# Kernel tuning notes

Measured on AMD Instinct MI355X. Metric: run time of the kernel, lower is better.

The kernel has to match this reference:

```python
import jax, jax.numpy as jnp
import numpy as np

N, HR, HEADS = 1024, 2048, 4
C1 = HR // HEADS                      # 512 per-head dim, conv1
H2 = 2 * HEADS                        # 8 heads, conv2
C2 = (2 * HR) // (2 * HEADS)          # 512 per-head dim, conv2
EPS = 1e-5


def setup_inputs() -> dict:
    key = jax.random.key(0)
    ks = jax.random.split(key, 20)
    s1 = 1.0 / np.sqrt(N)
    s2 = 1.0 / np.sqrt(HR)
    f32 = jnp.float32
    d = {"x": jax.random.normal(ks[0], (N, N), f32)}
    # conv1 params (in=N, out=HR)
    d["q1_w"] = jax.random.normal(ks[1], (N, HR), f32) * s1
    d["q1_b"] = jnp.zeros((HR,), f32)
    d["k1_w"] = jax.random.normal(ks[2], (N, HR), f32) * s1
    d["k1_b"] = jnp.zeros((HR,), f32)
    d["v1_w"] = jax.random.normal(ks[3], (N, HR), f32) * s1
    d["v1_b"] = jnp.zeros((HR,), f32)
    d["e1_w"] = jax.random.normal(ks[4], (HR,), f32) * 0.1   # lin_edge (edge_dim=1, no bias)
    d["s1_w"] = jax.random.normal(ks[5], (N, HR), f32) * s1  # lin_skip
    d["s1_b"] = jnp.zeros((HR,), f32)
    d["gn1_gamma"] = jnp.ones((HR,), f32)
    d["gn1_beta"] = jnp.zeros((HR,), f32)
    d["gn1_ms"] = jnp.ones((HR,), f32)
    # conv2 params (in=HR, out=2*HR)
    d["q2_w"] = jax.random.normal(ks[6], (HR, 2 * HR), f32) * s2
    d["q2_b"] = jnp.zeros((2 * HR,), f32)
    d["k2_w"] = jax.random.normal(ks[7], (HR, 2 * HR), f32) * s2
    d["k2_b"] = jnp.zeros((2 * HR,), f32)
    d["v2_w"] = jax.random.normal(ks[8], (HR, 2 * HR), f32) * s2
    d["v2_b"] = jnp.zeros((2 * HR,), f32)
    d["e2_w"] = jax.random.normal(ks[9], (2 * HR,), f32) * 0.1
    d["s2_w"] = jax.random.normal(ks[10], (HR, 2 * HR), f32) * s2
    d["s2_b"] = jnp.zeros((2 * HR,), f32)
    d["gn2_gamma"] = jnp.ones((2 * HR,), f32)
    d["gn2_beta"] = jnp.zeros((2 * HR,), f32)
    d["gn2_ms"] = jnp.ones((2 * HR,), f32)
    return d


def _tconv(x, A, qw, qb, kw, kb, vw, vb, ew, sw, sb, H, Cd):
    # TransformerConv over fully-connected meshgrid graph; edge (r -> c) carries scalar A[r, c].
    # key_j/value_j get +A[r,c]*We; the edge term factors out so no [N,N,H,C] tensor is built.
    n = x.shape[0]
    q = (x @ qw + qb).reshape(n, H, Cd)   # targets c
    k = (x @ kw + kb).reshape(n, H, Cd)   # sources r
    v = (x @ vw + vb).reshape(n, H, Cd)
    We = ew.reshape(H, Cd)
    qk = jnp.einsum('chd,rhd->crh', q, k)                 # [N_tgt, N_src, H]
    qe = jnp.einsum('chd,hd->ch', q, We)                  # q_c . We per head
    logits = (qk + A.T[:, :, None] * qe[:, None, :]) / jnp.sqrt(jnp.float32(Cd))
    alpha = jax.nn.softmax(logits, axis=1)                # softmax over sources per target
    out = jnp.einsum('crh,rhd->chd', alpha, v)
    out = out + jnp.einsum('crh,rc->ch', alpha, A)[:, :, None] * We[None]
    return out.reshape(n, H * Cd) + x @ sw + sb           # root/skip connection


def _gnorm(x, gamma, beta, ms):
    # GraphNorm over a single graph: learnable mean-scale, per-feature stats across nodes.
    mu = x.mean(axis=0)
    out = x - ms * mu
    var = (out * out).mean(axis=0)
    return gamma * out * jax.lax.rsqrt(var + EPS) + beta


def reference(x, q1_w, q1_b, k1_w, k1_b, v1_w, v1_b, e1_w, s1_w, s1_b,
              gn1_gamma, gn1_beta, gn1_ms,
              q2_w, q2_b, k2_w, k2_b, v2_w, v2_b, e2_w, s2_w, s2_b,
              gn2_gamma, gn2_beta, gn2_ms):
    A = x  # edge attrs are x.view(-1, 1) over the meshgrid edge_index
    h1 = _tconv(x, A, q1_w, q1_b, k1_w, k1_b, v1_w, v1_b, e1_w, s1_w, s1_b, HEADS, C1)
    h1 = _gnorm(h1, gn1_gamma, gn1_beta, gn1_ms)
    h2 = _tconv(h1, A, q2_w, q2_b, k2_w, k2_b, v2_w, v2_b, e2_w, s2_w, s2_b, H2, C2)
    h2 = _gnorm(h2, gn2_gamma, gn2_beta, gn2_ms)
    return h2 / jnp.linalg.norm(h2, axis=1, keepdims=True)
```

## Files before the change

kernel.cpp:

```cpp
#include <hip/hip_runtime.h>
#include <math.h>

#define EPSV 1e-5f

typedef __attribute__((ext_vector_type(8))) short bf16x8;
typedef __attribute__((ext_vector_type(4))) float f32x4;

__device__ __forceinline__ unsigned short f2bf(float f) {
    unsigned int u = __float_as_uint(f);
    return (unsigned short)((u + 0x7fffu + ((u >> 16) & 1u)) >> 16);
}
__device__ __forceinline__ float b2f(unsigned short u) {
    return __uint_as_float(((unsigned int)u) << 16);
}

__device__ __forceinline__ void glds16(const unsigned short* g, unsigned short* l) {
    __builtin_amdgcn_global_load_lds(
        (const __attribute__((address_space(1))) void*)g,
        (__attribute__((address_space(3))) void*)l, 16, 0, 0);
}

template<int BIAS, int OUTBF>
__global__ __launch_bounds__(256) void gemm_bt(
    const unsigned short* __restrict__ A, const unsigned short* __restrict__ B,
    const float* __restrict__ bias, void* __restrict__ Cout,
    int K, int lda, int ldb, int ldc,
    long aH, long bH, long cH)
{
    __shared__ unsigned short As[4096];
    __shared__ unsigned short Bs[4096];
    const int tid = threadIdx.x;
    const int wid = tid >> 6, lane = tid & 63;
    const int bm = blockIdx.y * 128, bn = blockIdx.x * 128;
    A += (long)blockIdx.z * aH;
    B += (long)blockIdx.z * bH;

    const int wr = wid >> 1, wc = wid & 1;

    const int r0 = (wid << 4) + (lane >> 2);
    const int kq = (lane & 3) << 3;
    const unsigned short* gA0 = A + (long)(bm + r0) * lda + kq;
    const unsigned short* gA1 = gA0 + (long)64 * lda;
    const unsigned short* gB0 = B + (long)(bn + r0) * ldb + kq;
    const unsigned short* gB1 = gB0 + (long)64 * ldb;
    unsigned short* lA0 = &As[wid << 9];
    unsigned short* lA1 = &As[(wid << 9) + 2048];
    unsigned short* lB0 = &Bs[wid << 9];
    unsigned short* lB1 = &Bs[(wid << 9) + 2048];

    f32x4 acc[4][4];
    #pragma unroll
    for (int m = 0; m < 4; m++)
        #pragma unroll
        for (int n = 0; n < 4; n++) acc[m][n] = (f32x4){0.f, 0.f, 0.f, 0.f};

    const int fr = lane & 15;
    const int kb = (lane >> 4) << 3;
    const unsigned short* pA = &As[(wr * 64 + fr) * 32 + kb];
    const unsigned short* pB = &Bs[(wc * 64 + fr) * 32 + kb];

    for (int k0 = 0; k0 < K; k0 += 32) {
        glds16(gA0 + k0, lA0);
        glds16(gA1 + k0, lA1);
        glds16(gB0 + k0, lB0);
        glds16(gB1 + k0, lB1);
        __syncthreads();
        bf16x8 af[4], bfr[4];
        #pragma unroll
        for (int m = 0; m < 4; m++) af[m] = *(const bf16x8*)(pA + (m << 9));
        #pragma unroll
        for (int n = 0; n < 4; n++) bfr[n] = *(const bf16x8*)(pB + (n << 9));
        #pragma unroll
        for (int m = 0; m < 4; m++)
            #pragma unroll
            for (int n = 0; n < 4; n++)
                acc[m][n] = __builtin_amdgcn_mfma_f32_16x16x32_bf16(
                    af[m], bfr[n], acc[m][n], 0, 0, 0);
        __syncthreads();
    }

    const int er = (lane >> 4) << 2;
    const int ec = lane & 15;
    if (OUTBF) {
        unsigned short* C = (unsigned short*)Cout + (long)blockIdx.z * cH;
        #pragma unroll
        for (int m = 0; m < 4; m++)
            #pragma unroll
            for (int n = 0; n < 4; n++) {
                int col = bn + wc * 64 + n * 16 + ec;
                float bv = BIAS ? bias[col] : 0.f;
                #pragma unroll
                for (int j = 0; j < 4; j++) {
                    int row = bm + wr * 64 + m * 16 + er + j;
                    C[(long)row * ldc + col] = f2bf(acc[m][n][j] + bv);
                }
            }
    } else {
        float* C = (float*)Cout + (long)blockIdx.z * cH;
        #pragma unroll
        for (int m = 0; m < 4; m++)
            #pragma unroll
            for (int n = 0; n < 4; n++) {
                int col = bn + wc * 64 + n * 16 + ec;
                #pragma unroll
                for (int j = 0; j < 4; j++) {
                    int row = bm + wr * 64 + m * 16 + er + j;
                    C[(long)row * ldc + col] = acc[m][n][j];
                }
            }
    }
}

__global__ void f2b_kernel(const float* __restrict__ src, unsigned short* __restrict__ dst)
{
    long i = ((long)blockIdx.x * 256 + threadIdx.x) * 8;
    float4 a = *(const float4*)&src[i];
    float4 b = *(const float4*)&src[i + 4];
    unsigned short o[8] = { f2bf(a.x), f2bf(a.y), f2bf(a.z), f2bf(a.w),
                            f2bf(b.x), f2bf(b.y), f2bf(b.z), f2bf(b.w) };
    *(uint4*)&dst[i] = *(uint4*)o;
}

__global__ void transpose_f2b(const float* __restrict__ src, unsigned short* __restrict__ dst,
                              int ldsrc, int Kdim)
{
    __shared__ float t[32][33];
    int f0 = blockIdx.x * 32, k0 = blockIdx.y * 32;
    int tx = threadIdx.x, ty = threadIdx.y;
    #pragma unroll
    for (int i = 0; i < 4; i++)
        t[ty + i * 8][tx] = src[(long)(k0 + ty + i * 8) * ldsrc + f0 + tx];
    __syncthreads();
    #pragma unroll
    for (int i = 0; i < 4; i++)
        dst[(long)(f0 + ty + i * 8) * Kdim + k0 + tx] = f2bf(t[tx][ty + i * 8]);
}

__global__ void transpose_b2b(const unsigned short* __restrict__ src,
                              unsigned short* __restrict__ dst, int ldsrc, int Cd)
{
    __shared__ unsigned short t[32][33];
    int h = blockIdx.z;
    int d0 = blockIdx.x * 32, r0 = blockIdx.y * 32;
    int tx = threadIdx.x, ty = threadIdx.y;
    #pragma unroll
    for (int i = 0; i < 4; i++)
        t[ty + i * 8][tx] = src[(long)(r0 + ty + i * 8) * ldsrc + h * Cd + d0 + tx];
    __syncthreads();
    #pragma unroll
    for (int i = 0; i < 4; i++)
        dst[(long)h * Cd * 1024 + (long)(d0 + ty + i * 8) * 1024 + r0 + tx] = t[tx][ty + i * 8];
}

__global__ void concat4(const float* __restrict__ a, const float* __restrict__ b,
                        const float* __restrict__ c, const float* __restrict__ d,
                        float* __restrict__ o, int F)
{
    int i = blockIdx.x * 256 + threadIdx.x;
    const float* s = (i < F) ? a : (i < 2 * F) ? b : (i < 3 * F) ? c : d;
    o[i] = s[i & (F - 1)];
}

__global__ void transpose1024(const float* __restrict__ in, float* __restrict__ out)
{
    __shared__ float t[32][33];
    int bx = blockIdx.x * 32, by = blockIdx.y * 32;
    #pragma unroll
    for (int i = 0; i < 32; i += 8)
        t[threadIdx.y + i][threadIdx.x] = in[(long)(by + threadIdx.y + i) * 1024 + bx + threadIdx.x];
    __syncthreads();
    #pragma unroll
    for (int i = 0; i < 32; i += 8)
        out[(long)(bx + threadIdx.y + i) * 1024 + by + threadIdx.x] = t[threadIdx.x][threadIdx.y + i];
}

__global__ __launch_bounds__(256) void compute_qe_b(
    const unsigned short* __restrict__ q, const float* __restrict__ ew,
    float* __restrict__ qe, int H, int Cd, int ldq)
{
    int gw = (blockIdx.x * 256 + threadIdx.x) >> 6;
    int lane = threadIdx.x & 63;
    int c = gw / H, h = gw - c * H;
    const unsigned short* qr = q + (long)c * ldq + h * Cd;
    const float* w = ew + h * Cd;
    int d = lane * 8;
    ushort4 u0 = *(const ushort4*)&qr[d];
    ushort4 u1 = *(const ushort4*)&qr[d + 4];
    float4 w0 = *(const float4*)&w[d];
    float4 w1 = *(const float4*)&w[d + 4];
    float s = b2f(u0.x) * w0.x + b2f(u0.y) * w0.y + b2f(u0.z) * w0.z + b2f(u0.w) * w0.w
            + b2f(u1.x) * w1.x + b2f(u1.y) * w1.y + b2f(u1.z) * w1.z + b2f(u1.w) * w1.w;
    #pragma unroll
    for (int o = 32; o; o >>= 1) s += __shfl_xor(s, o);
    if (lane == 0) qe[c * H + h] = s;
}

__global__ __launch_bounds__(256) void softmax_edge(
    const float* __restrict__ S, const float* __restrict__ xT,
    const float* __restrict__ qe, float* __restrict__ aw,
    unsigned short* __restrict__ ab, int H, float inv_sqrt_d)
{
    const int c = blockIdx.x, h = blockIdx.y, tid = threadIdx.x;
    const float* row = S + ((long)h * 1024 + c) * 1024;
    unsigned short* arow = ab + ((long)h * 1024 + c) * 1024;
    const float* xc = xT + (long)c * 1024;
    const float qeh = qe[c * H + h] * inv_sqrt_d;
    float l[4], xv[4];
    float mx = -1e30f;
    #pragma unroll
    for (int i = 0; i < 4; i++) {
        int r = tid + i * 256;
        xv[i] = xc[r];
        l[i] = row[r] * inv_sqrt_d + xv[i] * qeh;
        mx = fmaxf(mx, l[i]);
    }
    __shared__ float red[8];
    #pragma unroll
    for (int o = 32; o; o >>= 1) mx = fmaxf(mx, __shfl_xor(mx, o));
    if ((tid & 63) == 0) red[tid >> 6] = mx;
    __syncthreads();
    mx = fmaxf(fmaxf(red[0], red[1]), fmaxf(red[2], red[3]));
    __syncthreads();
    float e[4], se = 0.f, sa = 0.f;
    #pragma unroll
    for (int i = 0; i < 4; i++) {
        e[i] = __expf(l[i] - mx);
        se += e[i];
        sa += e[i] * xv[i];
    }
    #pragma unroll
    for (int o = 32; o; o >>= 1) { se += __shfl_xor(se, o); sa += __shfl_xor(sa, o); }
    if ((tid & 63) == 0) { red[tid >> 6] = se; red[4 + (tid >> 6)] = sa; }
    __syncthreads();
    se = red[0] + red[1] + red[2] + red[3];
    sa = red[4] + red[5] + red[6] + red[7];
    float inv = 1.f / se;
    #pragma unroll
    for (int i = 0; i < 4; i++) arow[tid + i * 256] = f2bf(e[i] * inv);
    if (tid == 0) aw[c * H + h] = sa * inv;
}

__global__ void combine2(float* __restrict__ out, const unsigned short* __restrict__ skipb,
                         int ldskip, const float* __restrict__ aw, const float* __restrict__ ew,
                         int F, int H)
{
    long idx = ((long)blockIdx.x * 256 + threadIdx.x) * 4;
    int c = (int)(idx / F), f = (int)(idx % F);
    int h = f >> 9;
    float a = aw[c * H + h];
    ushort4 sk = *(const ushort4*)&skipb[(long)c * ldskip + f];
    float4 o = *(float4*)&out[idx];
    float4 w = *(const float4*)&ew[f];
    o.x += b2f(sk.x) + a * w.x; o.y += b2f(sk.y) + a * w.y;
    o.z += b2f(sk.z) + a * w.z; o.w += b2f(sk.w) + a * w.w;
    *(float4*)&out[idx] = o;
}

__global__ void col_stats1(const float* __restrict__ X, float* __restrict__ ps,
                           float* __restrict__ ps2, int F)
{
    int f = blockIdx.x * 256 + threadIdx.x;
    int r0 = blockIdx.y * 32;
    float s = 0.f, s2 = 0.f;
    for (int r = r0; r < r0 + 32; r++) {
        float v = X[(long)r * F + f];
        s += v; s2 += v * v;
    }
    ps [(long)blockIdx.y * F + f] = s;
    ps2[(long)blockIdx.y * F + f] = s2;
}

__global__ void col_stats2(const float* __restrict__ ps, const float* __restrict__ ps2,
    const float* __restrict__ ms, float* __restrict__ msmu, float* __restrict__ rs, int F)
{
    int f = blockIdx.x * 256 + threadIdx.x;
    float s = 0.f, s2 = 0.f;
    for (int ch = 0; ch < 32; ch++) { s += ps[(long)ch * F + f]; s2 += ps2[(long)ch * F + f]; }
    float m  = s  * (1.f / 1024.f);
    float m2 = s2 * (1.f / 1024.f);
    float a = ms[f] * m;
    msmu[f] = a;
    float var = m2 - 2.f * a * m + a * a;
    rs[f] = rsqrtf(var + EPSV);
}

__global__ void gnorm_apply(float* __restrict__ X, const float* __restrict__ msmu,
    const float* __restrict__ rs, const float* __restrict__ g, const float* __restrict__ b, int F)
{
    long idx = ((long)blockIdx.x * 256 + threadIdx.x) * 4;
    int f = (int)(idx % F);
    float4 v = *(float4*)&X[idx];
    v.x = g[f+0] * (v.x - msmu[f+0]) * rs[f+0] + b[f+0];
    v.y = g[f+1] * (v.y - msmu[f+1]) * rs[f+1] + b[f+1];
    v.z = g[f+2] * (v.z - msmu[f+2]) * rs[f+2] + b[f+2];
    v.w = g[f+3] * (v.w - msmu[f+3]) * rs[f+3] + b[f+3];
    *(float4*)&X[idx] = v;
}

__global__ __launch_bounds__(256) void l2norm_rows(float* __restrict__ X, int F)
{
    const int r = blockIdx.x, tid = threadIdx.x;
    float* row = X + (long)r * F;
    float s = 0.f;
    for (int f = tid * 4; f < F; f += 1024) {
        float4 v = *(const float4*)&row[f];
        s += v.x*v.x + v.y*v.y + v.z*v.z + v.w*v.w;
    }
    __shared__ float red[4];
    #pragma unroll
    for (int o = 32; o; o >>= 1) s += __shfl_xor(s, o);
    if ((tid & 63) == 0) red[tid >> 6] = s;
    __syncthreads();
    s = red[0] + red[1] + red[2] + red[3];
    float inv = rsqrtf(s);
    for (int f = tid * 4; f < F; f += 1024) {
        float4 v = *(const float4*)&row[f];
        v.x *= inv; v.y *= inv; v.z *= inv; v.w *= inv;
        *(float4*)&row[f] = v;
    }
}

typedef unsigned short u16;

static inline void launch_gemm(hipStream_t st, const u16* A, const u16* B, const float* bias,
                               void* C, int M, int N, int K, int lda, int ldb, int ldc,
                               int nz, long aH, long bH, long cH, bool outbf)
{
    dim3 g(N / 128, M / 128, nz), b(256);
    if (outbf) {
        if (bias) gemm_bt<1,1><<<g, b, 0, st>>>(A, B, bias, C, K, lda, ldb, ldc, aH, bH, cH);
        else      gemm_bt<0,1><<<g, b, 0, st>>>(A, B, bias, C, K, lda, ldb, ldc, aH, bH, cH);
    } else {
        gemm_bt<0,0><<<g, b, 0, st>>>(A, B, bias, C, K, lda, ldb, ldc, aH, bH, cH);
    }
}

extern "C" void kernel_launch(void* const* d_in, const int* in_sizes, int n_in,
                              void* d_out, int out_size, void* d_ws, size_t ws_size,
                              hipStream_t stream)
{
    const float* x    = (const float*)d_in[0];
    const float* q1w  = (const float*)d_in[1];  const float* q1b = (const float*)d_in[2];
    const float* k1w  = (const float*)d_in[3];  const float* k1b = (const float*)d_in[4];
    const float* v1w  = (const float*)d_in[5];  const float* v1b = (const float*)d_in[6];
    const float* e1w  = (const float*)d_in[7];
    const float* s1w  = (const float*)d_in[8];  const float* s1b = (const float*)d_in[9];
    const float* gn1g = (const float*)d_in[10]; const float* gn1b = (const float*)d_in[11];
    const float* gn1ms= (const float*)d_in[12];
    const float* q2w  = (const float*)d_in[13]; const float* q2b = (const float*)d_in[14];
    const float* k2w  = (const float*)d_in[15]; const float* k2b = (const float*)d_in[16];
    const float* v2w  = (const float*)d_in[17]; const float* v2b = (const float*)d_in[18];
    const float* e2w  = (const float*)d_in[19];
    const float* s2w  = (const float*)d_in[20]; const float* s2b = (const float*)d_in[21];
    const float* gn2g = (const float*)d_in[22]; const float* gn2b = (const float*)d_in[23];
    const float* gn2ms= (const float*)d_in[24];
    float* out = (float*)d_out;

    char* W = (char*)d_ws;
    float* xT    = (float*)W;               W += (long)1024 * 1024 * 4;
    u16*   xb    = (u16*)W;                 W += (long)1024 * 1024 * 2;
    float* h1    = (float*)W;               W += (long)1024 * 2048 * 4;
    u16*   h1b   = (u16*)W;                 W += (long)1024 * 2048 * 2;
    u16*   projC = (u16*)W;                 W += (long)1024 * 16384 * 2;
    char*  R     = W;                       W += (long)8192 * 2048 * 2;
    u16*   WT    = (u16*)R;
    float* S     = (float*)R;
    u16*   ab    = (u16*)W;                 W += (long)8 * 1024 * 1024 * 2;
    u16*   VT    = (u16*)W;                 W += (long)8 * 512 * 1024 * 2;
    float* bc    = (float*)W;               W += 16384 * 4;
    float* qe    = (float*)W;               W += 8192 * 4;
    float* aw    = (float*)W;               W += 8192 * 4;
    float* ps    = (float*)W;               W += (long)32 * 4096 * 4;
    float* ps2   = (float*)W;               W += (long)32 * 4096 * 4;
    float* msmu  = (float*)W;               W += 4096 * 4;
    float* rs    = (float*)W;               W += 4096 * 4;

    const float isd = 1.0f / sqrtf(512.0f);

    transpose1024<<<dim3(32, 32), dim3(32, 8), 0, stream>>>(x, xT);
    f2b_kernel<<<512, 256, 0, stream>>>(x, xb);

    {
        const int F = 2048, K = 1024, H = 4;
        transpose_f2b<<<dim3(64, 32), dim3(32, 8), 0, stream>>>(q1w, WT + (long)0 * F * K, F, K);
        transpose_f2b<<<dim3(64, 32), dim3(32, 8), 0, stream>>>(k1w, WT + (long)1 * F * K, F, K);
        transpose_f2b<<<dim3(64, 32), dim3(32, 8), 0, stream>>>(v1w, WT + (long)2 * F * K, F, K);
        transpose_f2b<<<dim3(64, 32), dim3(32, 8), 0, stream>>>(s1w, WT + (long)3 * F * K, F, K);
        concat4<<<32, 256, 0, stream>>>(q1b, k1b, v1b, s1b, bc, F);
        launch_gemm(stream, xb, WT, bc, projC, 1024, 4 * F, K, K, K, 4 * F, 1, 0, 0, 0, true);

        compute_qe_b<<<1024, 256, 0, stream>>>(projC, e1w, qe, H, 512, 4 * F);
        launch_gemm(stream, projC, projC + F, nullptr, S, 1024, 1024, 512,
                    4 * F, 4 * F, 1024, H, 512, 512, (long)1024 * 1024, false);
        softmax_edge<<<dim3(1024, H), 256, 0, stream>>>(S, xT, qe, aw, ab, H, isd);
        transpose_b2b<<<dim3(16, 32, H), dim3(32, 8), 0, stream>>>(projC + 2 * F, VT, 4 * F, 512);
        launch_gemm(stream, ab, VT, nullptr, h1, 1024, 512, 1024,
                    1024, 1024, F, H, (long)1024 * 1024, (long)512 * 1024, 512, false);
        combine2<<<2048, 256, 0, stream>>>(h1, projC + 3 * F, 4 * F, aw, e1w, F, H);

        col_stats1<<<dim3(F / 256, 32), 256, 0, stream>>>(h1, ps, ps2, F);
        col_stats2<<<F / 256, 256, 0, stream>>>(ps, ps2, gn1ms, msmu, rs, F);
        gnorm_apply<<<(int)((long)1024 * F / 4 / 256), 256, 0, stream>>>(h1, msmu, rs, gn1g, gn1b, F);
    }
    f2b_kernel<<<1024, 256, 0, stream>>>(h1, h1b);

    {
        const int F = 4096, K = 2048, H = 8;
        concat4<<<64, 256, 0, stream>>>(q2b, k2b, v2b, s2b, bc, F);
        transpose_f2b<<<dim3(128, 64), dim3(32, 8), 0, stream>>>(q2w, WT + (long)0 * F * K, F, K);
        transpose_f2b<<<dim3(128, 64), dim3(32, 8), 0, stream>>>(k2w, WT + (long)1 * F * K, F, K);
        launch_gemm(stream, h1b, WT, bc, projC, 1024, 2 * F, K, K, K, 4 * F, 1, 0, 0, 0, true);
        transpose_f2b<<<dim3(128, 64), dim3(32, 8), 0, stream>>>(v2w, WT + (long)0 * F * K, F, K);
        transpose_f2b<<<dim3(128, 64), dim3(32, 8), 0, stream>>>(s2w, WT + (long)1 * F * K, F, K);
        launch_gemm(stream, h1b, WT, bc + 2 * F, projC + 2 * F, 1024, 2 * F, K, K, K, 4 * F, 1, 0, 0, 0, true);

        compute_qe_b<<<2048, 256, 0, stream>>>(projC, e2w, qe, H, 512, 4 * F);
        launch_gemm(stream, projC, projC + F, nullptr, S, 1024, 1024, 512,
                    4 * F, 4 * F, 1024, H, 512, 512, (long)1024 * 1024, false);
        softmax_edge<<<dim3(1024, H), 256, 0, stream>>>(S, xT, qe, aw, ab, H, isd);
        transpose_b2b<<<dim3(16, 32, H), dim3(32, 8), 0, stream>>>(projC + 2 * F, VT, 4 * F, 512);
        launch_gemm(stream, ab, VT, nullptr, out, 1024, 512, 1024,
                    1024, 1024, F, H, (long)1024 * 1024, (long)512 * 1024, 512, false);
        combine2<<<4096, 256, 0, stream>>>(out, projC + 3 * F, 4 * F, aw, e2w, F, H);

        col_stats1<<<dim3(F / 256, 32), 256, 0, stream>>>(out, ps, ps2, F);
        col_stats2<<<F / 256, 256, 0, stream>>>(ps, ps2, gn2ms, msmu, rs, F);
        gnorm_apply<<<(int)((long)1024 * F / 4 / 256), 256, 0, stream>>>(out, msmu, rs, gn2g, gn2b, F);
    }
    l2norm_rows<<<1024, 256, 0, stream>>>(out, 4096);
}
```

Measured before the change: 585.7 us.

## Replace GEMM with 256x128 triple-buffered swizzled kernel and fuse elementwise passes

Replaces the 128x128 single-buffered bf16 GEMM with a 512-thread 128x256 tile kernel. It uses BK=64, three LDS buffers with global_load_lds prefetch, XOR swizzling and raw barriers and waitcnts. Several small kernels are fused: the combine step goes into the PV GEMM epilogue, qe into the softmax, gnorm into the bf16 cast and into the L2 norm, the x transpose into the cast, and the four weight transposes into one launch. The goal is higher MFMA utilisation and fewer launches and memory passes, at the cost of large LDS use and hand-tuned synchronisation that could be fragile.

Result: faster. 472.4 us (-19.3%).

```diff
diff --git a/kernel.cpp b/kernel.cpp
--- a/kernel.cpp
+++ b/kernel.cpp
@@ -5,95 +5,147 @@
 
 typedef __attribute__((ext_vector_type(8))) short bf16x8;
 typedef __attribute__((ext_vector_type(4))) float f32x4;
-
-__device__ __forceinline__ unsigned short f2bf(float f) {
+typedef unsigned short u16;
+
+__device__ __forceinline__ u16 f2bf(float f) {
     unsigned int u = __float_as_uint(f);
-    return (unsigned short)((u + 0x7fffu + ((u >> 16) & 1u)) >> 16);
-}
-__device__ __forceinline__ float b2f(unsigned short u) {
+    return (u16)((u + 0x7fffu + ((u >> 16) & 1u)) >> 16);
+}
+__device__ __forceinline__ float b2f(u16 u) {
     return __uint_as_float(((unsigned int)u) << 16);
 }
 
-__device__ __forceinline__ void glds16(const unsigned short* g, unsigned short* l) {
+__device__ __forceinline__ void glds16(const u16* g, u16* l) {
     __builtin_amdgcn_global_load_lds(
         (const __attribute__((address_space(1))) void*)g,
         (__attribute__((address_space(3))) void*)l, 16, 0, 0);
 }
 
-template<int BIAS, int OUTBF>
-__global__ __launch_bounds__(256) void gemm_bt(
-    const unsigned short* __restrict__ A, const unsigned short* __restrict__ B,
+#define BARRIER() asm volatile("s_barrier" ::: "memory")
+#define VMCNT(n)  asm volatile("s_waitcnt vmcnt(" #n ")" ::: "memory")
+
+template<int BIAS, int OUTBF, int PVEPI>
+__global__ __launch_bounds__(512, 2) void gemm256(
+    const u16* __restrict__ A, const u16* __restrict__ B,
     const float* __restrict__ bias, void* __restrict__ Cout,
-    int K, int lda, int ldb, int ldc,
-    long aH, long bH, long cH)
-{
-    __shared__ unsigned short As[4096];
-    __shared__ unsigned short Bs[4096];
+    int K, int lda, int ldb, int ldc, long aH, long bH, long cH,
+    const u16* __restrict__ skipb, int ldsk,
+    const float* __restrict__ aw, const float* __restrict__ ew, int H)
+{
+    __shared__ __align__(16) u16 LB[3 * 24576];
     const int tid = threadIdx.x;
     const int wid = tid >> 6, lane = tid & 63;
-    const int bm = blockIdx.y * 128, bn = blockIdx.x * 128;
-    A += (long)blockIdx.z * aH;
-    B += (long)blockIdx.z * bH;
-
-    const int wr = wid >> 1, wc = wid & 1;
-
-    const int r0 = (wid << 4) + (lane >> 2);
-    const int kq = (lane & 3) << 3;
-    const unsigned short* gA0 = A + (long)(bm + r0) * lda + kq;
-    const unsigned short* gA1 = gA0 + (long)64 * lda;
-    const unsigned short* gB0 = B + (long)(bn + r0) * ldb + kq;
-    const unsigned short* gB1 = gB0 + (long)64 * ldb;
-    unsigned short* lA0 = &As[wid << 9];
-    unsigned short* lA1 = &As[(wid << 9) + 2048];
-    unsigned short* lB0 = &Bs[wid << 9];
-    unsigned short* lB1 = &Bs[(wid << 9) + 2048];
-
+    const int wm = wid >> 2, wn = wid & 3;
+    const int fr = lane & 15, g = lane >> 4;
+    const int bm = blockIdx.y * 128, bn = blockIdx.x * 256;
+    if (PVEPI) { A += (long)(bn >> 9) * aH; }
+    else       { A += (long)blockIdx.z * aH; B += (long)blockIdx.z * bH; }
+
+    const int srow = tid >> 3;
+    const int kx = ((tid & 7) ^ (srow & 7)) << 3;
+    const u16* gA = A + (long)(bm + srow) * lda + kx;
+    const u16* gB = B + (long)(bn + srow) * ldb + kx;
+
+#define STAGEA(dst, tt) do { const u16* s_ = gA + ((long)(tt) << 6); \
+    u16* d_ = (dst) + (wid << 9); \
+    glds16(s_, d_); glds16(s_ + (long)64 * lda, d_ + 4096); } while (0)
+#define STAGEB(dst, tt) do { const u16* s_ = gB + ((long)(tt) << 6); \
+    u16* d_ = (dst) + 8192 + (wid << 9); \
+    glds16(s_, d_); \
+    glds16(s_ + (long)64 * ldb, d_ + 4096); \
+    glds16(s_ + (long)128 * ldb, d_ + 8192); \
+    glds16(s_ + (long)192 * ldb, d_ + 12288); } while (0)
+
+    const int q0 = ((0 + g) ^ (fr & 7)) << 3;
+    const int q1 = ((4 + g) ^ (fr & 7)) << 3;
+    bf16x8 am[4], bq[4];
     f32x4 acc[4][4];
     #pragma unroll
     for (int m = 0; m < 4; m++)
         #pragma unroll
         for (int n = 0; n < 4; n++) acc[m][n] = (f32x4){0.f, 0.f, 0.f, 0.f};
 
-    const int fr = lane & 15;
-    const int kb = (lane >> 4) << 3;
-    const unsigned short* pA = &As[(wr * 64 + fr) * 32 + kb];
-    const unsigned short* pB = &Bs[(wc * 64 + fr) * 32 + kb];
-
-    for (int k0 = 0; k0 < K; k0 += 32) {
-        glds16(gA0 + k0, lA0);
-        glds16(gA1 + k0, lA1);
-        glds16(gB0 + k0, lB0);
-        glds16(gB1 + k0, lB1);
-        __syncthreads();
-        bf16x8 af[4], bfr[4];
-        #pragma unroll
-        for (int m = 0; m < 4; m++) af[m] = *(const bf16x8*)(pA + (m << 9));
-        #pragma unroll
-        for (int n = 0; n < 4; n++) bfr[n] = *(const bf16x8*)(pB + (n << 9));
-        #pragma unroll
-        for (int m = 0; m < 4; m++)
-            #pragma unroll
-            for (int n = 0; n < 4; n++)
-                acc[m][n] = __builtin_amdgcn_mfma_f32_16x16x32_bf16(
-                    af[m], bfr[n], acc[m][n], 0, 0, 0);
-        __syncthreads();
-    }
-
-    const int er = (lane >> 4) << 2;
-    const int ec = lane & 15;
-    if (OUTBF) {
-        unsigned short* C = (unsigned short*)Cout + (long)blockIdx.z * cH;
+#define RD8(bp, qq) do { \
+    const u16* pa_ = (bp) + ((wm << 6) + fr) * 64; \
+    const u16* pb_ = (bp) + 8192 + ((wn << 6) + fr) * 64; \
+    am[0] = *(const bf16x8*)(pa_ + (qq)); \
+    am[1] = *(const bf16x8*)(pa_ + 1024 + (qq)); \
+    am[2] = *(const bf16x8*)(pa_ + 2048 + (qq)); \
+    am[3] = *(const bf16x8*)(pa_ + 3072 + (qq)); \
+    bq[0] = *(const bf16x8*)(pb_ + (qq)); \
+    bq[1] = *(const bf16x8*)(pb_ + 1024 + (qq)); \
+    bq[2] = *(const bf16x8*)(pb_ + 2048 + (qq)); \
+    bq[3] = *(const bf16x8*)(pb_ + 3072 + (qq)); } while (0)
+
+#define MFMA16() do { __builtin_amdgcn_s_setprio(1); \
+    _Pragma("unroll") for (int m_ = 0; m_ < 4; m_++) \
+    _Pragma("unroll") for (int n_ = 0; n_ < 4; n_++) \
+        acc[m_][n_] = __builtin_amdgcn_mfma_f32_16x16x32_bf16(am[m_], bq[n_], acc[m_][n_], 0, 0, 0); \
+    __builtin_amdgcn_s_setprio(0); } while (0)
+
+    u16* pr = LB;
+    u16* pn = LB + 24576;
+    u16* ps = LB + 49152;
+
+    STAGEA(pr, 0); STAGEB(pr, 0);
+    STAGEA(pn, 1); STAGEB(pn, 1);
+    VMCNT(6);
+    BARRIER();
+
+    const int NT = K >> 6;
+    for (int t = 0; t < NT - 2; ++t) {
+        RD8(pr, q0);
+        STAGEA(ps, t + 2);
+        BARRIER();
+        MFMA16();
+        BARRIER();
+        RD8(pr, q1);
+        STAGEB(ps, t + 2);
+        VMCNT(6);
+        BARRIER();
+        MFMA16();
+        BARRIER();
+        u16* tmp = pr; pr = pn; pn = ps; ps = tmp;
+    }
+    RD8(pr, q0); BARRIER(); MFMA16(); BARRIER();
+    RD8(pr, q1);
+    VMCNT(0);
+    BARRIER();
+    MFMA16();
+    RD8(pn, q0); MFMA16();
+    RD8(pn, q1); MFMA16();
+
+    const int er = g << 2;
+    const int crow0 = bm + (wm << 6);
+    const int ccol0 = bn + (wn << 6);
+    if (PVEPI) {
+        float* C = (float*)Cout;
         #pragma unroll
         for (int m = 0; m < 4; m++)
             #pragma unroll
             for (int n = 0; n < 4; n++) {
-                int col = bn + wc * 64 + n * 16 + ec;
+                int f = ccol0 + (n << 4) + fr;
+                int h = f >> 9;
+                float ewf = ew[f];
+                #pragma unroll
+                for (int j = 0; j < 4; j++) {
+                    int row = crow0 + (m << 4) + er + j;
+                    C[(long)row * ldc + f] = acc[m][n][j]
+                        + b2f(skipb[(long)row * ldsk + f])
+                        + aw[row * H + h] * ewf;
+                }
+            }
+    } else if (OUTBF) {
+        u16* C = (u16*)Cout + (long)blockIdx.z * cH;
+        #pragma unroll
+        for (int m = 0; m < 4; m++)
+            #pragma unroll
+            for (int n = 0; n < 4; n++) {
+                int col = ccol0 + (n << 4) + fr;
                 float bv = BIAS ? bias[col] : 0.f;
                 #pragma unroll
-                for (int j = 0; j < 4; j++) {
-                    int row = bm + wr * 64 + m * 16 + er + j;
-                    C[(long)row * ldc + col] = f2bf(acc[m][n][j] + bv);
-                }
+                for (int j = 0; j < 4; j++)
+                    C[(long)(crow0 + (m << 4) + er + j) * ldc + col] = f2bf(acc[m][n][j] + bv);
             }
     } else {
         float* C = (float*)Cout + (long)blockIdx.z * cH;
@@ -101,29 +153,41 @@
         for (int m = 0; m < 4; m++)
             #pragma unroll
             for (int n = 0; n < 4; n++) {
-                int col = bn + wc * 64 + n * 16 + ec;
+                int col = ccol0 + (n << 4) + fr;
                 #pragma unroll
-                for (int j = 0; j < 4; j++) {
-                    int row = bm + wr * 64 + m * 16 + er + j;
-                    C[(long)row * ldc + col] = acc[m][n][j];
-                }
+                for (int j = 0; j < 4; j++)
+                    C[(long)(crow0 + (m << 4) + er + j) * ldc + col] = acc[m][n][j];
             }
     }
-}
-
-__global__ void f2b_kernel(const float* __restrict__ src, unsigned short* __restrict__ dst)
-{
-    long i = ((long)blockIdx.x * 256 + threadIdx.x) * 8;
-    float4 a = *(const float4*)&src[i];
-    float4 b = *(const float4*)&src[i + 4];
-    unsigned short o[8] = { f2bf(a.x), f2bf(a.y), f2bf(a.z), f2bf(a.w),
-                            f2bf(b.x), f2bf(b.y), f2bf(b.z), f2bf(b.w) };
-    *(uint4*)&dst[i] = *(uint4*)o;
-}
-
-__global__ void transpose_f2b(const float* __restrict__ src, unsigned short* __restrict__ dst,
-                              int ldsrc, int Kdim)
-{
+#undef STAGEA
+#undef STAGEB
+#undef RD8
+#undef MFMA16
+}
+
+__global__ void xprep(const float* __restrict__ in, float* __restrict__ outT,
+                      u16* __restrict__ outB)
+{
+    __shared__ float t[32][33];
+    int bx = blockIdx.x * 32, by = blockIdx.y * 32;
+    #pragma unroll
+    for (int i = 0; i < 32; i += 8) {
+        float v = in[(long)(by + threadIdx.y + i) * 1024 + bx + threadIdx.x];
+        t[threadIdx.y + i][threadIdx.x] = v;
+        outB[(long)(by + threadIdx.y + i) * 1024 + bx + threadIdx.x] = f2bf(v);
+    }
+    __syncthreads();
+    #pragma unroll
+    for (int i = 0; i < 32; i += 8)
+        outT[(long)(bx + threadIdx.y + i) * 1024 + by + threadIdx.x] = t[threadIdx.x][threadIdx.y + i];
+}
+
+__global__ void wtrans4(const float* s0, const float* s1, const float* s2, const float* s3,
+                        u16* __restrict__ dst, int ldsrc, int Kdim, long dstride)
+{
+    int which = blockIdx.z;
+    const float* src = which == 0 ? s0 : which == 1 ? s1 : which == 2 ? s2 : s3;
+    dst += (long)which * dstride;
     __shared__ float t[32][33];
     int f0 = blockIdx.x * 32, k0 = blockIdx.y * 32;
     int tx = threadIdx.x, ty = threadIdx.y;
@@ -136,10 +200,10 @@
         dst[(long)(f0 + ty + i * 8) * Kdim + k0 + tx] = f2bf(t[tx][ty + i * 8]);
 }
 
-__global__ void transpose_b2b(const unsigned short* __restrict__ src,
-                              unsigned short* __restrict__ dst, int ldsrc, int Cd)
-{
-    __shared__ unsigned short t[32][33];
+__global__ void transpose_b2b(const u16* __restrict__ src,
+                              u16* __restrict__ dst, int ldsrc, int Cd)
+{
+    __shared__ u16 t[32][33];
     int h = blockIdx.z;
     int d0 = blockIdx.x * 32, r0 = blockIdx.y * 32;
     int tx = threadIdx.x, ty = threadIdx.y;
@@ -161,60 +225,36 @@
     o[i] = s[i & (F - 1)];
 }
 
-__global__ void transpose1024(const float* __restrict__ in, float* __restrict__ out)
-{
-    __shared__ float t[32][33];
-    int bx = blockIdx.x * 32, by = blockIdx.y * 32;
-    #pragma unroll
-    for (int i = 0; i < 32; i += 8)
-        t[threadIdx.y + i][threadIdx.x] = in[(long)(by + threadIdx.y + i) * 1024 + bx + threadIdx.x];
-    __syncthreads();
-    #pragma unroll
-    for (int i = 0; i < 32; i += 8)
-        out[(long)(bx + threadIdx.y + i) * 1024 + by + threadIdx.x] = t[threadIdx.x][threadIdx.y + i];
-}
-
-__global__ __launch_bounds__(256) void compute_qe_b(
-    const unsigned short* __restrict__ q, const float* __restrict__ ew,
-    float* __restrict__ qe, int H, int Cd, int ldq)
-{
-    int gw = (blockIdx.x * 256 + threadIdx.x) >> 6;
-    int lane = threadIdx.x & 63;
-    int c = gw / H, h = gw - c * H;
-    const unsigned short* qr = q + (long)c * ldq + h * Cd;
-    const float* w = ew + h * Cd;
-    int d = lane * 8;
-    ushort4 u0 = *(const ushort4*)&qr[d];
-    ushort4 u1 = *(const ushort4*)&qr[d + 4];
-    float4 w0 = *(const float4*)&w[d];
-    float4 w1 = *(const float4*)&w[d + 4];
-    float s = b2f(u0.x) * w0.x + b2f(u0.y) * w0.y + b2f(u0.z) * w0.z + b2f(u0.w) * w0.w
-            + b2f(u1.x) * w1.x + b2f(u1.y) * w1.y + b2f(u1.z) * w1.z + b2f(u1.w) * w1.w;
-    #pragma unroll
-    for (int o = 32; o; o >>= 1) s += __shfl_xor(s, o);
-    if (lane == 0) qe[c * H + h] = s;
-}
-
-__global__ __launch_bounds__(256) void softmax_edge(
+__global__ __launch_bounds__(256) void softmax_qe(
     const float* __restrict__ S, const float* __restrict__ xT,
-    const float* __restrict__ qe, float* __restrict__ aw,
-    unsigned short* __restrict__ ab, int H, float inv_sqrt_d)
+    const u16* __restrict__ qmat, int ldq, const float* __restrict__ ew,
+    float* __restrict__ aw, u16* __restrict__ ab, int H, float isd)
 {
     const int c = blockIdx.x, h = blockIdx.y, tid = threadIdx.x;
+    __shared__ float red[8];
+    const u16* qr = qmat + (long)c * ldq + (h << 9);
+    const float* wv = ew + (h << 9);
+    int d = tid << 1;
+    float p = b2f(qr[d]) * wv[d] + b2f(qr[d + 1]) * wv[d + 1];
+    #pragma unroll
+    for (int o = 32; o; o >>= 1) p += __shfl_xor(p, o);
+    if ((tid & 63) == 0) red[tid >> 6] = p;
+    __syncthreads();
+    const float qeh = (red[0] + red[1] + red[2] + red[3]) * isd;
+    __syncthreads();
+
     const float* row = S + ((long)h * 1024 + c) * 1024;
-    unsigned short* arow = ab + ((long)h * 1024 + c) * 1024;
+    u16* arow = ab + ((long)h * 1024 + c) * 1024;
     const float* xc = xT + (long)c * 1024;
-    const float qeh = qe[c * H + h] * inv_sqrt_d;
     float l[4], xv[4];
     float mx = -1e30f;
     #pragma unroll
     for (int i = 0; i < 4; i++) {
         int r = tid + i * 256;
         xv[i] = xc[r];
-        l[i] = row[r] * inv_sqrt_d + xv[i] * qeh;
+        l[i] = row[r] * isd + xv[i] * qeh;
         mx = fmaxf(mx, l[i]);
     }
-    __shared__ float red[8];
     #pragma unroll
     for (int o = 32; o; o >>= 1) mx = fmaxf(mx, __shfl_xor(mx, o));
     if ((tid & 63) == 0) red[tid >> 6] = mx;
@@ -238,22 +278,6 @@
     #pragma unroll
     for (int i = 0; i < 4; i++) arow[tid + i * 256] = f2bf(e[i] * inv);
     if (tid == 0) aw[c * H + h] = sa * inv;
-}
-
-__global__ void combine2(float* __restrict__ out, const unsigned short* __restrict__ skipb,
-                         int ldskip, const float* __restrict__ aw, const float* __restrict__ ew,
-                         int F, int H)
-{
-    long idx = ((long)blockIdx.x * 256 + threadIdx.x) * 4;
-    int c = (int)(idx / F), f = (int)(idx % F);
-    int h = f >> 9;
-    float a = aw[c * H + h];
-    ushort4 sk = *(const ushort4*)&skipb[(long)c * ldskip + f];
-    float4 o = *(float4*)&out[idx];
-    float4 w = *(const float4*)&ew[f];
-    o.x += b2f(sk.x) + a * w.x; o.y += b2f(sk.y) + a * w.y;
-    o.z += b2f(sk.z) + a * w.z; o.w += b2f(sk.w) + a * w.w;
-    *(float4*)&out[idx] = o;
 }
 
 __global__ void col_stats1(const float* __restrict__ X, float* __restrict__ ps,
@@ -284,55 +308,81 @@
     rs[f] = rsqrtf(var + EPSV);
 }
 
-__global__ void gnorm_apply(float* __restrict__ X, const float* __restrict__ msmu,
-    const float* __restrict__ rs, const float* __restrict__ g, const float* __restrict__ b, int F)
+__global__ void gnorm_apply_b(const float* __restrict__ X, u16* __restrict__ Yb,
+    const float* __restrict__ msmu, const float* __restrict__ rs,
+    const float* __restrict__ g, const float* __restrict__ b, int F)
 {
     long idx = ((long)blockIdx.x * 256 + threadIdx.x) * 4;
     int f = (int)(idx % F);
-    float4 v = *(float4*)&X[idx];
+    float4 v = *(const float4*)&X[idx];
     v.x = g[f+0] * (v.x - msmu[f+0]) * rs[f+0] + b[f+0];
     v.y = g[f+1] * (v.y - msmu[f+1]) * rs[f+1] + b[f+1];
     v.z = g[f+2] * (v.z - msmu[f+2]) * rs[f+2] + b[f+2];
     v.w = g[f+3] * (v.w - msmu[f+3]) * rs[f+3] + b[f+3];
-    *(float4*)&X[idx] = v;
-}
-
-__global__ __launch_bounds__(256) void l2norm_rows(float* __restrict__ X, int F)
+    u16 o[4] = { f2bf(v.x), f2bf(v.y), f2bf(v.z), f2bf(v.w) };
+    *(ushort4*)&Yb[idx] = *(ushort4*)o;
+}
+
+__global__ __launch_bounds__(256) void gnorm_l2(
+    float* __restrict__ X, const float* __restrict__ msmu,
+    const float* __restrict__ rs, const float* __restrict__ g,
+    const float* __restrict__ b, int F)
 {
     const int r = blockIdx.x, tid = threadIdx.x;
     float* row = X + (long)r * F;
-    float s = 0.f;
-    for (int f = tid * 4; f < F; f += 1024) {
-        float4 v = *(const float4*)&row[f];
-        s += v.x*v.x + v.y*v.y + v.z*v.z + v.w*v.w;
+    float v[16];
+    float ss = 0.f;
+    #pragma unroll
+    for (int i = 0; i < 4; i++) {
+        int f = (tid << 2) + (i << 10);
+        float4 x4 = *(const float4*)&row[f];
+        float a0 = g[f+0] * (x4.x - msmu[f+0]) * rs[f+0] + b[f+0];
+        float a1 = g[f+1] * (x4.y - msmu[f+1]) * rs[f+1] + b[f+1];
+        float a2 = g[f+2] * (x4.z - msmu[f+2]) * rs[f+2] + b[f+2];
+        float a3 = g[f+3] * (x4.w - msmu[f+3]) * rs[f+3] + b[f+3];
+        v[i*4+0] = a0; v[i*4+1] = a1; v[i*4+2] = a2; v[i*4+3] = a3;
+        ss += a0*a0 + a1*a1 + a2*a2 + a3*a3;
     }
     __shared__ float red[4];
     #pragma unroll
-    for (int o = 32; o; o >>= 1) s += __shfl_xor(s, o);
-    if ((tid & 63) == 0) red[tid >> 6] = s;
-    __syncthreads();
-    s = red[0] + red[1] + red[2] + red[3];
-    float inv = rsqrtf(s);
-    for (int f = tid * 4; f < F; f += 1024) {
-        float4 v = *(const float4*)&row[f];
-        v.x *= inv; v.y *= inv; v.z *= inv; v.w *= inv;
-        *(float4*)&row[f] = v;
-    }
-}
-
-typedef unsigned short u16;
-
-static inline void launch_gemm(hipStream_t st, const u16* A, const u16* B, const float* bias,
-                               void* C, int M, int N, int K, int lda, int ldb, int ldc,
-                               int nz, long aH, long bH, long cH, bool outbf)
-{
-    dim3 g(N / 128, M / 128, nz), b(256);
-    if (outbf) {
-        if (bias) gemm_bt<1,1><<<g, b, 0, st>>>(A, B, bias, C, K, lda, ldb, ldc, aH, bH, cH);
-        else      gemm_bt<0,1><<<g, b, 0, st>>>(A, B, bias, C, K, lda, ldb, ldc, aH, bH, cH);
-    } else {
-        gemm_bt<0,0><<<g, b, 0, st>>>(A, B, bias, C, K, lda, ldb, ldc, aH, bH, cH);
-    }
+    for (int o = 32; o; o >>= 1) ss += __shfl_xor(ss, o);
+    if ((tid & 63) == 0) red[tid >> 6] = ss;
+    __syncthreads();
+    ss = red[0] + red[1] + red[2] + red[3];
+    float inv = rsqrtf(ss);
+    #pragma unroll
+    for (int i = 0; i < 4; i++) {
+        int f = (tid << 2) + (i << 10);
+        float4 o4;
+        o4.x = v[i*4+0] * inv; o4.y = v[i*4+1] * inv;
+        o4.z = v[i*4+2] * inv; o4.w = v[i*4+3] * inv;
+        *(float4*)&row[f] = o4;
+    }
+}
+
+static inline void g256_proj(hipStream_t st, const u16* A, const u16* B, const float* bias,
+                             u16* C, int M, int N, int K, int lda, int ldb, int ldc)
+{
+    dim3 gr(N / 256, M / 128, 1), bl(512);
+    gemm256<1,1,0><<<gr, bl, 0, st>>>(A, B, bias, C, K, lda, ldb, ldc, 0, 0, 0,
+                                      nullptr, 0, nullptr, nullptr, 0);
+}
+static inline void g256_qk(hipStream_t st, const u16* A, const u16* B, float* C,
+                           int K, int lda, int ldb, int H)
+{
+    dim3 gr(1024 / 256, 1024 / 128, H), bl(512);
+    gemm256<0,0,0><<<gr, bl, 0, st>>>(A, B, nullptr, C, K, lda, ldb, 1024,
+                                      512, 512, (long)1024 * 1024,
+                                      nullptr, 0, nullptr, nullptr, 0);
+}
+static inline void g256_pv(hipStream_t st, const u16* A, const u16* B, float* C,
+                           int H, int F, const u16* skipb, int ldsk,
+                           const float* aw, const float* ew)
+{
+    dim3 gr((H * 512) / 256, 1024 / 128, 1), bl(512);
+    gemm256<0,0,1><<<gr, bl, 0, st>>>(A, B, nullptr, C, 1024, 1024, 1024, F,
+                                      (long)1024 * 1024, 0, 0,
+                                      skipb, ldsk, aw, ew, H);
 }
 
 extern "C" void kernel_launch(void* const* d_in, const int* in_sizes, int n_in,
@@ -368,7 +418,6 @@
     u16*   ab    = (u16*)W;                 W += (long)8 * 1024 * 1024 * 2;
     u16*   VT    = (u16*)W;                 W += (long)8 * 512 * 1024 * 2;
     float* bc    = (float*)W;               W += 16384 * 4;
-    float* qe    = (float*)W;               W += 8192 * 4;
     float* aw    = (float*)W;               W += 8192 * 4;
     float* ps    = (float*)W;               W += (long)32 * 4096 * 4;
     float* ps2   = (float*)W;               W += (long)32 * 4096 * 4;
@@ -377,55 +426,42 @@
 
     const float isd = 1.0f / sqrtf(512.0f);
 
-    transpose1024<<<dim3(32, 32), dim3(32, 8), 0, stream>>>(x, xT);
-    f2b_kernel<<<512, 256, 0, stream>>>(x, xb);
+    xprep<<<dim3(32, 32), dim3(32, 8), 0, stream>>>(x, xT, xb);
 
     {
         const int F = 2048, K = 1024, H = 4;
-        transpose_f2b<<<dim3(64, 32), dim3(32, 8), 0, stream>>>(q1w, WT + (long)0 * F * K, F, K);
-        transpose_f2b<<<dim3(64, 32), dim3(32, 8), 0, stream>>>(k1w, WT + (long)1 * F * K, F, K);
-        transpose_f2b<<<dim3(64, 32), dim3(32, 8), 0, stream>>>(v1w, WT + (long)2 * F * K, F, K);
-        transpose_f2b<<<dim3(64, 32), dim3(32, 8), 0, stream>>>(s1w, WT + (long)3 * F * K, F, K);
+        wtrans4<<<dim3(64, 32, 4), dim3(32, 8), 0, stream>>>(
+            q1w, k1w, v1w, s1w, WT, F, K, (long)F * K);
         concat4<<<32, 256, 0, stream>>>(q1b, k1b, v1b, s1b, bc, F);
-        launch_gemm(stream, xb, WT, bc, projC, 1024, 4 * F, K, K, K, 4 * F, 1, 0, 0, 0, true);
-
-        compute_qe_b<<<1024, 256, 0, stream>>>(projC, e1w, qe, H, 512, 4 * F);
-        launch_gemm(stream, projC, projC + F, nullptr, S, 1024, 1024, 512,
-                    4 * F, 4 * F, 1024, H, 512, 512, (long)1024 * 1024, false);
-        softmax_edge<<<dim3(1024, H), 256, 0, stream>>>(S, xT, qe, aw, ab, H, isd);
+        g256_proj(stream, xb, WT, bc, projC, 1024, 4 * F, K, K, K, 4 * F);
+        g256_qk(stream, projC, projC + F, S, 512, 4 * F, 4 * F, H);
+        softmax_qe<<<dim3(1024, H), 256, 0, stream>>>(S, xT, projC, 4 * F, e1w, aw, ab, H, isd);
         transpose_b2b<<<dim3(16, 32, H), dim3(32, 8), 0, stream>>>(projC + 2 * F, VT, 4 * F, 512);
-        launch_gemm(stream, ab, VT, nullptr, h1, 1024, 512, 1024,
-                    1024, 1024, F, H, (long)1024 * 1024, (long)512 * 1024, 512, false);
-        combine2<<<2048, 256, 0, stream>>>(h1, projC + 3 * F, 4 * F, aw, e1w, F, H);
+        g256_pv(stream, ab, VT, h1, H, F, projC + 3 * F, 4 * F, aw, e1w);
 
         col_stats1<<<dim3(F / 256, 32), 256, 0, stream>>>(h1, ps, ps2, F);
         col_stats2<<<F / 256, 256, 0, stream>>>(ps, ps2, gn1ms, msmu, rs, F);
-        gnorm_apply<<<(int)((long)1024 * F / 4 / 256), 256, 0, stream>>>(h1, msmu, rs, gn1g, gn1b, F);
-    }
-    f2b_kernel<<<1024, 256, 0, stream>>>(h1, h1b);
+        gnorm_apply_b<<<(int)((long)1024 * F / 4 / 256), 256, 0, stream>>>(
+            h1, h1b, msmu, rs, gn1g, gn1b, F);
+    }
 
     {
         const int F = 4096, K = 2048, H = 8;
         concat4<<<64, 256, 0, stream>>>(q2b, k2b, v2b, s2b, bc, F);
-        transpose_f2b<<<dim3(128, 64), dim3(32, 8), 0, stream>>>(q2w, WT + (long)0 * F * K, F, K);
-        transpose_f2b<<<dim3(128, 64), dim3(32, 8), 0, stream>>>(k2w, WT + (long)1 * F * K, F, K);
-        launch_gemm(stream, h1b, WT, bc, projC, 1024, 2 * F, K, K, K, 4 * F, 1, 0, 0, 0, true);
-        transpose_f2b<<<dim3(128, 64), dim3(32, 8), 0, stream>>>(v2w, WT + (long)0 * F * K, F, K);
-        transpose_f2b<<<dim3(128, 64), dim3(32, 8), 0, stream>>>(s2w, WT + (long)1 * F * K, F, K);
-        launch_gemm(stream, h1b, WT, bc + 2 * F, projC + 2 * F, 1024, 2 * F, K, K, K, 4 * F, 1, 0, 0, 0, true);
-
-        compute_qe_b<<<2048, 256, 0, stream>>>(projC, e2w, qe, H, 512, 4 * F);
-        launch_gemm(stream, projC, projC + F, nullptr, S, 1024, 1024, 512,
-                    4 * F, 4 * F, 1024, H, 512, 512, (long)1024 * 1024, false);
-        softmax_edge<<<dim3(1024, H), 256, 0, stream>>>(S, xT, qe, aw, ab, H, isd);
+        wtrans4<<<dim3(128, 64, 2), dim3(32, 8), 0, stream>>>(
+            q2w, k2w, nullptr, nullptr, WT, F, K, (long)F * K);
+        g256_proj(stream, h1b, WT, bc, projC, 1024, 2 * F, K, K, K, 4 * F);
+        wtrans4<<<dim3(128, 64, 2), dim3(32, 8), 0, stream>>>(
+            v2w, s2w, nullptr, nullptr, WT, F, K, (long)F * K);
+        g256_proj(stream, h1b, WT, bc + 2 * F, projC + 2 * F, 1024, 2 * F, K, K, K, 4 * F);
+
+        g256_qk(stream, projC, projC + F, S, 512, 4 * F, 4 * F, H);
+        softmax_qe<<<dim3(1024, H), 256, 0, stream>>>(S, xT, projC, 4 * F, e2w, aw, ab, H, isd);
         transpose_b2b<<<dim3(16, 32, H), dim3(32, 8), 0, stream>>>(projC + 2 * F, VT, 4 * F, 512);
-        launch_gemm(stream, ab, VT, nullptr, out, 1024, 512, 1024,
-                    1024, 1024, F, H, (long)1024 * 1024, (long)512 * 1024, 512, false);
-        combine2<<<4096, 256, 0, stream>>>(out, projC + 3 * F, 4 * F, aw, e2w, F, H);
+        g256_pv(stream, ab, VT, out, H, F, projC + 3 * F, 4 * F, aw, e2w);
 
         col_stats1<<<dim3(F / 256, 32), 256, 0, stream>>>(out, ps, ps2, F);
         col_stats2<<<F / 256, 256, 0, stream>>>(ps, ps2, gn2ms, msmu, rs, F);
-        gnorm_apply<<<(int)((long)1024 * F / 4 / 256), 256, 0, stream>>>(out, msmu, rs, gn2g, gn2b, F);
-    }
-    l2norm_rows<<<1024, 256, 0, stream>>>(out, 4096);
-}
+        gnorm_l2<<<1024, 256, 0, stream>>>(out, msmu, rs, gn2g, gn2b, F);
+    }
+}
```
